# Kernel tuning notes

Measured on AMD Instinct MI355X. Metric: run time of the kernel, lower is better.

Reference implementation:

```python
import jax, jax.numpy as jnp
import numpy as np

N = 100000   # nodes
E = 1280000  # edges (avg degree ~12.8)
D = 64       # feature / hidden channels


def _init_linear(key, fan_in, fan_out):
    # Kaiming-uniform-ish init like torch Linear
    bound = 1.0 / np.sqrt(fan_in)
    return jax.random.uniform(key, (fan_in, fan_out), minval=-bound, maxval=bound)


def setup_inputs() -> dict:
    key = jax.random.key(0)
    ks = jax.random.split(key, 16)
    inp = {
        "x": jax.random.normal(ks[0], (N, D), dtype=jnp.float32),
        "edge_index": jax.random.randint(ks[1], (2, E), 0, N, dtype=jnp.int32),
        "edge_weight": jax.random.uniform(ks[2], (E,), dtype=jnp.float32),
        "batch": jnp.zeros((N,), dtype=jnp.int32),
    }
    # GraphConv params per layer: lin_rel (weight+bias) applied to aggregated
    # neighbor sum, lin_root (weight, no bias) applied to the node itself.
    for i, k in zip((1, 2, 3), range(3, 12, 3)):
        inp[f"W_rel{i}"] = _init_linear(ks[k], D, D)
        inp[f"b_rel{i}"] = jnp.zeros((D,), dtype=jnp.float32)
        inp[f"W_root{i}"] = _init_linear(ks[k + 1], D, D)
    return inp


def _graph_conv(x, src, dst, w, W_rel, b_rel, W_root):
    # message: w_ij * x_j, aggregated (sum) at target nodes
    msg = w[:, None] * x[src]                                  # [E, D]
    agg = jax.ops.segment_sum(msg, dst, num_segments=N)       # [N, D]
    return agg @ W_rel + b_rel + x @ W_root                   # [N, D]


def reference(x, edge_index, edge_weight, batch,
              W_rel1, b_rel1, W_root1,
              W_rel2, b_rel2, W_root2,
              W_rel3, b_rel3, W_root3):
    src, dst = edge_index[0], edge_index[1]
    h = jax.nn.relu(_graph_conv(x, src, dst, edge_weight, W_rel1, b_rel1, W_root1))
    h = jax.nn.relu(_graph_conv(h, src, dst, edge_weight, W_rel2, b_rel2, W_root2))
    h = _graph_conv(h, src, dst, edge_weight, W_rel3, b_rel3, W_root3)
    return h
```

## Files before the change

### kernel.cpp

```cpp
#include <hip/hip_runtime.h>
#include <hip/hip_bf16.h>

#define NN 100000
#define NE 1280000
#define DD 64
#define RSHIFT 9
#define NRANGE 196
#define NPAD (NRANGE * 512)

typedef __attribute__((ext_vector_type(8))) short bf16x8;
typedef __attribute__((ext_vector_type(4))) float f32x4;

static __device__ __forceinline__ unsigned short f2bf(float f) {
    __hip_bfloat16 h = __float2bfloat16(f);
    return *reinterpret_cast<unsigned short*>(&h);
}

__global__ __launch_bounds__(256) void f32_to_bf16_kernel(
    const float* __restrict__ in, unsigned short* __restrict__ out)
{
    int i = (blockIdx.x * 256 + threadIdx.x) * 4;
    float4 v = *(const float4*)(in + i);
    ushort4 o;
    o.x = f2bf(v.x); o.y = f2bf(v.y); o.z = f2bf(v.z); o.w = f2bf(v.w);
    *(ushort4*)(out + i) = o;
}

__global__ __launch_bounds__(256) void bpack_kernel(
    const float* __restrict__ Wrel1, const float* __restrict__ Wroot1,
    const float* __restrict__ Wrel2, const float* __restrict__ Wroot2,
    const float* __restrict__ Wrel3, const float* __restrict__ Wroot3,
    unsigned short* __restrict__ Bp)
{
    int L = blockIdx.x;
    const float* Wrel  = (L == 0) ? Wrel1  : (L == 1) ? Wrel2  : Wrel3;
    const float* Wroot = (L == 0) ? Wroot1 : (L == 1) ? Wroot2 : Wroot3;
    int tid = threadIdx.x;
    int wv = tid >> 6, lane = tid & 63, quad = lane >> 4, m16 = lane & 15;
    int n = wv * 16 + m16;
    unsigned short* o = Bp + (size_t)L * 4 * 256 * 8;
#pragma unroll
    for (int t = 0; t < 4; ++t)
#pragma unroll
        for (int j = 0; j < 8; ++j) {
            int k = t * 32 + quad * 8 + j;
            float wval = (k < 64) ? Wrel[k * 64 + n] : Wroot[(k - 64) * 64 + n];
            o[((size_t)t * 256 + tid) * 8 + j] = f2bf(wval);
        }
}

__global__ __launch_bounds__(256) void hist2_kernel(
    const int* __restrict__ dst, int* __restrict__ rangeCnt)
{
    __shared__ int h[256];
    int tid = threadIdx.x;
    h[tid] = 0;
    __syncthreads();
    int e0 = blockIdx.x * 1024 + tid * 4;
    int4 d4 = *(const int4*)(dst + e0);
    atomicAdd(&h[d4.x >> RSHIFT], 1);
    atomicAdd(&h[d4.y >> RSHIFT], 1);
    atomicAdd(&h[d4.z >> RSHIFT], 1);
    atomicAdd(&h[d4.w >> RSHIFT], 1);
    __syncthreads();
    if (tid < NRANGE && h[tid]) atomicAdd(&rangeCnt[tid], h[tid]);
}

__global__ __launch_bounds__(256) void scan196_kernel(
    const int* __restrict__ rangeCnt, int* __restrict__ rangeBase,
    int* __restrict__ gcur, int* __restrict__ rowptr)
{
    __shared__ int sd[256];
    int tid = threadIdx.x;
    int v = (tid < NRANGE) ? rangeCnt[tid] : 0;
    sd[tid] = v;
    __syncthreads();
    for (int o = 1; o < 256; o <<= 1) {
        int t = (tid >= o) ? sd[tid - o] : 0;
        __syncthreads();
        sd[tid] += t;
        __syncthreads();
    }
    if (tid < NRANGE) { int ex = sd[tid] - v; rangeBase[tid] = ex; gcur[tid] = ex; }
    if (tid == 0) { rangeBase[NRANGE] = NE; rowptr[NN] = NE; }
}

__global__ __launch_bounds__(512) void p1_bin_kernel(
    const int* __restrict__ src, const int* __restrict__ dst,
    const float* __restrict__ w, int* __restrict__ gcur,
    int2* __restrict__ ecoarse)
{
    __shared__ int2 stage[1024];
    __shared__ unsigned char sbkt[1024];
    __shared__ int cnt[256], ofs[256], gpos[256];
    __shared__ int wsum[4];

    int tid = threadIdx.x;
    int e0 = blockIdx.x * 1024 + tid * 2;
    int2   s2 = *(const int2*)(src + e0);
    int2   d2 = *(const int2*)(dst + e0);
    float2 w2 = *(const float2*)(w + e0);

    if (tid < 256) cnt[tid] = 0;
    __syncthreads();

    int ss[2] = {s2.x, s2.y};
    int dd[2] = {d2.x, d2.y};
    float ww[2] = {w2.x, w2.y};
    int b[2], p[2];
#pragma unroll
    for (int i = 0; i < 2; ++i) {
        b[i] = dd[i] >> RSHIFT;
        p[i] = atomicAdd(&cnt[b[i]], 1);
    }
    __syncthreads();

    if (tid < 256) {
        int v = cnt[tid];
        int lane6 = tid & 63;
        int sum = v;
#pragma unroll
        for (int o = 1; o < 64; o <<= 1) {
            int t = __shfl_up(sum, o);
            if (lane6 >= o) sum += t;
        }
        if (lane6 == 63) wsum[tid >> 6] = sum;
        ofs[tid] = sum - v;
    }
    __syncthreads();
    if (tid < 256) {
        int wid = tid >> 6;
        int pre = 0;
#pragma unroll
        for (int k = 0; k < 3; ++k) pre += (k < wid) ? wsum[k] : 0;
        ofs[tid] += pre;
        int cv = cnt[tid];
        if (tid < NRANGE && cv > 0) gpos[tid] = atomicAdd(&gcur[tid], cv);
    }
    __syncthreads();

#pragma unroll
    for (int i = 0; i < 2; ++i) {
        int slot = ofs[b[i]] + p[i];
        stage[slot] = make_int2(ss[i] | ((dd[i] & 511) << 17), __float_as_int(ww[i]));
        sbkt[slot] = (unsigned char)b[i];
    }
    __syncthreads();

#pragma unroll
    for (int u = 0; u < 2; ++u) {
        int j = tid + u * 512;
        int bb = sbkt[j];
        ecoarse[gpos[bb] + (j - ofs[bb])] = stage[j];
    }
}

__global__ __launch_bounds__(1024) void p2_place_kernel(
    const int2* __restrict__ ecoarse, const int* __restrict__ rangeBase,
    int* __restrict__ rowptr, int2* __restrict__ ebuf)
{
    __shared__ int cnt[512];
    __shared__ int wsum[8];
    int r = blockIdx.x, tid = threadIdx.x;
    int beg = rangeBase[r], end = rangeBase[r + 1];

    if (tid < 512) cnt[tid] = 0;
    __syncthreads();

    for (int j = beg + tid; j < end; j += 1024) {
        int2 rec = ecoarse[j];
        atomicAdd(&cnt[(rec.x >> 17) & 511], 1);
    }
    __syncthreads();

    int v = 0, sum = 0;
    if (tid < 512) {
        v = cnt[tid]; sum = v;
        int lane6 = tid & 63;
#pragma unroll
        for (int o = 1; o < 64; o <<= 1) {
            int t = __shfl_up(sum, o);
            if (lane6 >= o) sum += t;
        }
        if (lane6 == 63) wsum[tid >> 6] = sum;
    }
    __syncthreads();
    if (tid < 512) {
        int wid = tid >> 6;
        int pre = 0;
#pragma unroll
        for (int k = 0; k < 7; ++k) pre += (k < wid) ? wsum[k] : 0;
        int ex = beg + pre + sum - v;
        rowptr[(r << RSHIFT) + tid] = ex;
        cnt[tid] = ex;
    }
    __syncthreads();

    for (int j = beg + tid; j < end; j += 1024) {
        int2 rec = ecoarse[j];
        int dl = (rec.x >> 17) & 511;
        int pp = atomicAdd(&cnt[dl], 1);
        ebuf[pp] = make_int2(rec.x & 0x1FFFF, rec.y);
    }
}

template <bool RELU, bool OUT32>
__global__ __launch_bounds__(512) void fused_layer_kernel(
    const unsigned short* __restrict__ hb,
    const int* __restrict__ rowptr,
    const int2* __restrict__ ebuf,
    const unsigned short* __restrict__ Bp,
    const float* __restrict__ brel,
    void* __restrict__ outp)
{
    __shared__ __align__(16) unsigned int AstW[4 * 256];

    int tid = threadIdx.x;
    int lane = tid & 63;
    int wv = tid >> 6;
    int half = lane >> 5;
    int ch = lane & 31;
    int base = blockIdx.x * 16;
    int node = base + wv * 2 + half;

    const unsigned int* __restrict__ hw = (const unsigned int*)hb;

    bf16x8 bfrag[4];
    float bias = 0.f;
    if (wv < 4) {
#pragma unroll
        for (int t2 = 0; t2 < 4; ++t2)
            bfrag[t2] = *(const bf16x8*)(Bp + ((size_t)t2 * 256 + tid) * 8);
        bias = brel[(wv << 4) | (lane & 15)];
    }

    unsigned rootp = hw[(size_t)node * 32 + ch];

    int beg = rowptr[node];
    int end = rowptr[node + 1];
    int deg = end - beg;

    float aL[4] = {0.f, 0.f, 0.f, 0.f};
    float aH[4] = {0.f, 0.f, 0.f, 0.f};
    for (int c = 0; c < deg; c += 32) {
        int rem = deg - c;
        int nsl = rem < 32 ? rem : 32;
        int idx = (ch < nsl) ? (c + ch) : c;
        int2 e = ebuf[beg + idx];
        float wt = (ch < nsl) ? __int_as_float(e.y) : 0.f;

        for (int s0 = 0; s0 < nsl; s0 += 16) {
#pragma unroll
            for (int i = 0; i < 16; ++i) {
                int slot = s0 + i;
                bool ok = slot < nsl;
                int sl = (half << 5) | (ok ? slot : 0);
                int sr = __shfl(e.x, sl);
                float w = __shfl(wt, sl);
                w = ok ? w : 0.f;
                unsigned v = hw[(size_t)sr * 32 + ch];
                aL[i & 3] = fmaf(w, __uint_as_float(v << 16), aL[i & 3]);
                aH[i & 3] = fmaf(w, __uint_as_float(v & 0xFFFF0000u), aH[i & 3]);
            }
        }
    }
    float accL = (aL[0] + aL[1]) + (aL[2] + aL[3]);
    float accH = (aH[0] + aH[1]) + (aH[2] + aH[3]);

    int m = wv * 2 + half;
    int t = ch >> 4, q = (ch >> 2) & 3, jj = ch & 3;
    unsigned pack = ((unsigned)f2bf(accH) << 16) | (unsigned)f2bf(accL);
    AstW[t * 256 + (q * 16 + m) * 4 + jj] = pack;
    AstW[(2 + t) * 256 + (q * 16 + m) * 4 + jj] = rootp;
    __syncthreads();

    if (wv < 4) {
        int quad = lane >> 4, m16 = lane & 15;
        int n = wv * 16 + m16;
        f32x4 cacc = {0.f, 0.f, 0.f, 0.f};
#pragma unroll
        for (int t2 = 0; t2 < 4; ++t2) {
            bf16x8 a = *(const bf16x8*)&AstW[t2 * 256 + lane * 4];
            cacc = __builtin_amdgcn_mfma_f32_16x16x32_bf16(a, bfrag[t2], cacc, 0, 0, 0);
        }
#pragma unroll
        for (int reg = 0; reg < 4; ++reg) {
            int row = quad * 4 + reg;
            size_t onode = (size_t)base + row;
            float v2 = cacc[reg] + bias;
            if (RELU) v2 = fmaxf(v2, 0.f);
            if (OUT32) ((float*)outp)[onode * DD + n] = v2;
            else       ((unsigned short*)outp)[onode * DD + n] = f2bf(v2);
        }
    }
}

extern "C" void kernel_launch(void* const* d_in, const int* in_sizes, int n_in,
                              void* d_out, int out_size, void* d_ws, size_t ws_size,
                              hipStream_t stream)
{
    const float* x     = (const float*)d_in[0];
    const int*   ei    = (const int*)d_in[1];
    const float* w     = (const float*)d_in[2];
    const float* Wrel1 = (const float*)d_in[4];
    const float* brel1 = (const float*)d_in[5];
    const float* Wroot1= (const float*)d_in[6];
    const float* Wrel2 = (const float*)d_in[7];
    const float* brel2 = (const float*)d_in[8];
    const float* Wroot2= (const float*)d_in[9];
    const float* Wrel3 = (const float*)d_in[10];
    const float* brel3 = (const float*)d_in[11];
    const float* Wroot3= (const float*)d_in[12];

    float* out = (float*)d_out;

    char* ws = (char*)d_ws;
    int2*  ebuf    = (int2*)ws;                ws += (size_t)NE * 8;
    int2*  ecoarse = (int2*)ws;
    unsigned short* xb  = (unsigned short*)ws; ws += (size_t)NN * DD * 2;
    unsigned short* hb1 = (unsigned short*)ws; ws += (size_t)NN * DD * 2;
    unsigned short* hb2 = (unsigned short*)ws; ws += (size_t)NN * DD * 2;
    int*   rowptr = (int*)ws;                  ws += (size_t)(NPAD + 16) * 4;
    int*   rangeCnt  = (int*)ws;               ws += (size_t)256 * 4;
    int*   rangeBase = (int*)ws;               ws += (size_t)256 * 4;
    int*   gcur      = (int*)ws;               ws += (size_t)256 * 4;
    unsigned short* Bp = (unsigned short*)ws;

    const int* src = ei;
    const int* dst = ei + NE;

    hipMemsetAsync(rangeCnt, 0, NRANGE * 4, stream);
    bpack_kernel<<<3, 256, 0, stream>>>(Wrel1, Wroot1, Wrel2, Wroot2, Wrel3, Wroot3, Bp);
    hist2_kernel<<<1250, 256, 0, stream>>>(dst, rangeCnt);
    scan196_kernel<<<1, 256, 0, stream>>>(rangeCnt, rangeBase, gcur, rowptr);
    p1_bin_kernel<<<1250, 512, 0, stream>>>(src, dst, w, gcur, ecoarse);
    p2_place_kernel<<<NRANGE, 1024, 0, stream>>>(ecoarse, rangeBase, rowptr, ebuf);

    f32_to_bf16_kernel<<<6250, 256, 0, stream>>>(x, xb);

    fused_layer_kernel<true, false><<<NN / 16, 512, 0, stream>>>(
        xb, rowptr, ebuf, Bp, brel1, hb1);
    fused_layer_kernel<true, false><<<NN / 16, 512, 0, stream>>>(
        hb1, rowptr, ebuf, Bp + (size_t)4 * 256 * 8, brel2, hb2);
    fused_layer_kernel<false, true><<<NN / 16, 512, 0, stream>>>(
        hb2, rowptr, ebuf, Bp + (size_t)8 * 256 * 8, brel3, out);
}
```

Before: 309.0 us.

## Map one node per wave with scalar edge-record loads in fused layer

Each wave now aggregates a single node instead of two half-wave nodes, and block size grows to 1024 threads. Edge records are loaded as wave-uniform values via readfirstlane, replacing lane-distributed loads plus shuffles. This aims to cut shuffle and index overhead in the gather loop. In exchange, the upper 32 lanes do redundant work and twice as many waves are launched, which may reduce effective gather throughput.

```diff
diff --git a/kernel.cpp b/kernel.cpp
--- a/kernel.cpp
+++ b/kernel.cpp
@@ -205,7 +205,7 @@
 }
 
 template <bool RELU, bool OUT32>
-__global__ __launch_bounds__(512) void fused_layer_kernel(
+__global__ __launch_bounds__(1024) void fused_layer_kernel(
     const unsigned short* __restrict__ hb,
     const int* __restrict__ rowptr,
     const int2* __restrict__ ebuf,
@@ -218,10 +218,9 @@
     int tid = threadIdx.x;
     int lane = tid & 63;
     int wv = tid >> 6;
-    int half = lane >> 5;
     int ch = lane & 31;
     int base = blockIdx.x * 16;
-    int node = base + wv * 2 + half;
+    int node = base + wv;
 
     const unsigned int* __restrict__ hw = (const unsigned int*)hb;
 
@@ -236,42 +235,41 @@
 
     unsigned rootp = hw[(size_t)node * 32 + ch];
 
-    int beg = rowptr[node];
-    int end = rowptr[node + 1];
+    int beg = __builtin_amdgcn_readfirstlane(rowptr[node]);
+    int end = __builtin_amdgcn_readfirstlane(rowptr[node + 1]);
     int deg = end - beg;
+    const int2* __restrict__ erp = ebuf + beg;
 
     float aL[4] = {0.f, 0.f, 0.f, 0.f};
     float aH[4] = {0.f, 0.f, 0.f, 0.f};
-    for (int c = 0; c < deg; c += 32) {
-        int rem = deg - c;
-        int nsl = rem < 32 ? rem : 32;
-        int idx = (ch < nsl) ? (c + ch) : c;
-        int2 e = ebuf[beg + idx];
-        float wt = (ch < nsl) ? __int_as_float(e.y) : 0.f;
-
-        for (int s0 = 0; s0 < nsl; s0 += 16) {
-#pragma unroll
-            for (int i = 0; i < 16; ++i) {
-                int slot = s0 + i;
-                bool ok = slot < nsl;
-                int sl = (half << 5) | (ok ? slot : 0);
-                int sr = __shfl(e.x, sl);
-                float w = __shfl(wt, sl);
-                w = ok ? w : 0.f;
-                unsigned v = hw[(size_t)sr * 32 + ch];
-                aL[i & 3] = fmaf(w, __uint_as_float(v << 16), aL[i & 3]);
-                aH[i & 3] = fmaf(w, __uint_as_float(v & 0xFFFF0000u), aH[i & 3]);
-            }
+    for (int c = 0; c < deg; c += 8) {
+        int2 rec[8];
+#pragma unroll
+        for (int i = 0; i < 8; ++i) {
+            int j = c + i;
+            if (j >= deg) j = deg - 1;
+            rec[i] = erp[j];
+        }
+#pragma unroll
+        for (int i = 0; i < 8; ++i) {
+            int srcN  = __builtin_amdgcn_readfirstlane(rec[i].x);
+            int wbits = __builtin_amdgcn_readfirstlane(rec[i].y);
+            float w = (c + i < deg) ? __int_as_float(wbits) : 0.f;
+            unsigned v = hw[(size_t)srcN * 32 + ch];
+            aL[i & 3] = fmaf(w, __uint_as_float(v << 16), aL[i & 3]);
+            aH[i & 3] = fmaf(w, __uint_as_float(v & 0xFFFF0000u), aH[i & 3]);
         }
     }
     float accL = (aL[0] + aL[1]) + (aL[2] + aL[3]);
     float accH = (aH[0] + aH[1]) + (aH[2] + aH[3]);
 
-    int m = wv * 2 + half;
+    int m = wv;
     int t = ch >> 4, q = (ch >> 2) & 3, jj = ch & 3;
-    unsigned pack = ((unsigned)f2bf(accH) << 16) | (unsigned)f2bf(accL);
-    AstW[t * 256 + (q * 16 + m) * 4 + jj] = pack;
-    AstW[(2 + t) * 256 + (q * 16 + m) * 4 + jj] = rootp;
+    if (lane < 32) {
+        unsigned pack = ((unsigned)f2bf(accH) << 16) | (unsigned)f2bf(accL);
+        AstW[t * 256 + (q * 16 + m) * 4 + jj] = pack;
+        AstW[(2 + t) * 256 + (q * 16 + m) * 4 + jj] = rootp;
+    }
     __syncthreads();
 
     if (wv < 4) {
@@ -338,10 +336,10 @@
 
     f32_to_bf16_kernel<<<6250, 256, 0, stream>>>(x, xb);
 
-    fused_layer_kernel<true, false><<<NN / 16, 512, 0, stream>>>(
+    fused_layer_kernel<true, false><<<NN / 16, 1024, 0, stream>>>(
         xb, rowptr, ebuf, Bp, brel1, hb1);
-    fused_layer_kernel<true, false><<<NN / 16, 512, 0, stream>>>(
+    fused_layer_kernel<true, false><<<NN / 16, 1024, 0, stream>>>(
         hb1, rowptr, ebuf, Bp + (size_t)4 * 256 * 8, brel2, hb2);
-    fused_layer_kernel<false, true><<<NN / 16, 512, 0, stream>>>(
+    fused_layer_kernel<false, true><<<NN / 16, 1024, 0, stream>>>(
         hb2, rowptr, ebuf, Bp + (size_t)8 * 256 * 8, brel3, out);
 }
```

Result: slower. 329.5 us (+6.6%).

## Stage block edge lists in LDS and pre-scale source indices

Applied to the files above, without the earlier changes.

Each block of 16 nodes now cooperatively loads its contiguous edge records (up to 640) into shared memory, and each half-wave reads them with LDS broadcasts instead of per-chunk global loads plus cross-lane shuffles. Source indices are pre-multiplied by 32 during CSR construction so the gather address needs no multiply. Edges beyond the shared-memory capacity or leftover tails fall back to direct global reads. This adds a block barrier and extra LDS usage, which may lower occupancy.

```diff
diff --git a/kernel.cpp b/kernel.cpp
--- a/kernel.cpp
+++ b/kernel.cpp
@@ -7,6 +7,7 @@
 #define RSHIFT 9
 #define NRANGE 196
 #define NPAD (NRANGE * 512)
+#define SECAP 640
 
 typedef __attribute__((ext_vector_type(8))) short bf16x8;
 typedef __attribute__((ext_vector_type(4))) float f32x4;
@@ -200,7 +201,7 @@
         int2 rec = ecoarse[j];
         int dl = (rec.x >> 17) & 511;
         int pp = atomicAdd(&cnt[dl], 1);
-        ebuf[pp] = make_int2(rec.x & 0x1FFFF, rec.y);
+        ebuf[pp] = make_int2((rec.x & 0x1FFFF) << 5, rec.y);
     }
 }
 
@@ -214,6 +215,7 @@
     void* __restrict__ outp)
 {
     __shared__ __align__(16) unsigned int AstW[4 * 256];
+    __shared__ __align__(16) int2 se[SECAP];
 
     int tid = threadIdx.x;
     int lane = tid & 63;
@@ -225,6 +227,12 @@
 
     const unsigned int* __restrict__ hw = (const unsigned int*)hb;
 
+    int ebeg = __builtin_amdgcn_readfirstlane(rowptr[base]);
+    int eend = __builtin_amdgcn_readfirstlane(rowptr[base + 16]);
+    int ecnt = eend - ebeg;
+    int scnt = ecnt < SECAP ? ecnt : SECAP;
+    for (int j = tid; j < scnt; j += 512) se[j] = ebuf[ebeg + j];
+
     bf16x8 bfrag[4];
     float bias = 0.f;
     if (wv < 4) {
@@ -239,29 +247,38 @@
     int beg = rowptr[node];
     int end = rowptr[node + 1];
     int deg = end - beg;
+    int labeg = beg - ebeg;
+
+    __syncthreads();
 
     float aL[4] = {0.f, 0.f, 0.f, 0.f};
     float aH[4] = {0.f, 0.f, 0.f, 0.f};
-    for (int c = 0; c < deg; c += 32) {
-        int rem = deg - c;
-        int nsl = rem < 32 ? rem : 32;
-        int idx = (ch < nsl) ? (c + ch) : c;
-        int2 e = ebuf[beg + idx];
-        float wt = (ch < nsl) ? __int_as_float(e.y) : 0.f;
-
-        for (int s0 = 0; s0 < nsl; s0 += 16) {
-#pragma unroll
-            for (int i = 0; i < 16; ++i) {
-                int slot = s0 + i;
-                bool ok = slot < nsl;
-                int sl = (half << 5) | (ok ? slot : 0);
-                int sr = __shfl(e.x, sl);
-                float w = __shfl(wt, sl);
-                w = ok ? w : 0.f;
-                unsigned v = hw[(size_t)sr * 32 + ch];
-                aL[i & 3] = fmaf(w, __uint_as_float(v << 16), aL[i & 3]);
-                aH[i & 3] = fmaf(w, __uint_as_float(v & 0xFFFF0000u), aH[i & 3]);
-            }
+
+    int c = 0;
+    for (; c + 16 <= deg && labeg + c + 16 <= scnt; c += 16) {
+        int lb = labeg + c;
+        int2 rec[16];
+#pragma unroll
+        for (int i = 0; i < 16; ++i) rec[i] = se[lb + i];
+#pragma unroll
+        for (int i = 0; i < 16; ++i) {
+            float w = __int_as_float(rec[i].y);
+            unsigned v = hw[rec[i].x + ch];
+            aL[i & 3] = fmaf(w, __uint_as_float(v << 16), aL[i & 3]);
+            aH[i & 3] = fmaf(w, __uint_as_float(v & 0xFFFF0000u), aH[i & 3]);
+        }
+    }
+
+    for (; c < deg; c += 16) {
+#pragma unroll
+        for (int i = 0; i < 16; ++i) {
+            int j = c + i;
+            bool ok = j < deg;
+            int2 rec = ebuf[beg + (ok ? j : c)];
+            float w = ok ? __int_as_float(rec.y) : 0.f;
+            unsigned v = hw[rec.x + ch];
+            aL[i & 3] = fmaf(w, __uint_as_float(v << 16), aL[i & 3]);
+            aH[i & 3] = fmaf(w, __uint_as_float(v & 0xFFFF0000u), aH[i & 3]);
         }
     }
     float accL = (aL[0] + aL[1]) + (aL[2] + aL[3]);
```

Measured after the change: 446.1 us. 44.4% more time.

## Use finer 256-node bins and stage pre-scaled edge records in LDS for gather

Applied to the files above, without the earlier changes.

The coarse binning now uses 392 ranges of 256 nodes instead of 196 ranges of 512. The second placement pass runs with 512 threads per block and twice as many blocks, which raises parallelism in the CSR build. Edge source indices are stored pre-multiplied by the 128-byte row stride, and each wave stages its 32-edge chunk in shared memory instead of using two shuffles per neighbor. This removes per-edge multiply and shuffle work from the gather loop, at the cost of extra LDS traffic and more bins in the histogram and scan kernels.

```diff
diff --git a/kernel.cpp b/kernel.cpp
--- a/kernel.cpp
+++ b/kernel.cpp
@@ -4,9 +4,9 @@
 #define NN 100000
 #define NE 1280000
 #define DD 64
-#define RSHIFT 9
-#define NRANGE 196
-#define NPAD (NRANGE * 512)
+#define RSHIFT 8
+#define NRANGE 392
+#define NPAD (NRANGE * 256)
 
 typedef __attribute__((ext_vector_type(8))) short bf16x8;
 typedef __attribute__((ext_vector_type(4))) float f32x4;
@@ -49,12 +49,13 @@
         }
 }
 
-__global__ __launch_bounds__(256) void hist2_kernel(
+__global__ __launch_bounds__(256) void hist392_kernel(
     const int* __restrict__ dst, int* __restrict__ rangeCnt)
 {
-    __shared__ int h[256];
-    int tid = threadIdx.x;
-    h[tid] = 0;
+    __shared__ int h[NRANGE];
+    int tid = threadIdx.x;
+    if (tid < NRANGE) h[tid] = 0;
+    if (tid + 256 < NRANGE) h[tid + 256] = 0;
     __syncthreads();
     int e0 = blockIdx.x * 1024 + tid * 4;
     int4 d4 = *(const int4*)(dst + e0);
@@ -64,18 +65,19 @@
     atomicAdd(&h[d4.w >> RSHIFT], 1);
     __syncthreads();
     if (tid < NRANGE && h[tid]) atomicAdd(&rangeCnt[tid], h[tid]);
-}
-
-__global__ __launch_bounds__(256) void scan196_kernel(
+    if (tid + 256 < NRANGE && h[tid + 256]) atomicAdd(&rangeCnt[tid + 256], h[tid + 256]);
+}
+
+__global__ __launch_bounds__(512) void scan392_kernel(
     const int* __restrict__ rangeCnt, int* __restrict__ rangeBase,
     int* __restrict__ gcur, int* __restrict__ rowptr)
 {
-    __shared__ int sd[256];
+    __shared__ int sd[512];
     int tid = threadIdx.x;
     int v = (tid < NRANGE) ? rangeCnt[tid] : 0;
     sd[tid] = v;
     __syncthreads();
-    for (int o = 1; o < 256; o <<= 1) {
+    for (int o = 1; o < 512; o <<= 1) {
         int t = (tid >= o) ? sd[tid - o] : 0;
         __syncthreads();
         sd[tid] += t;
@@ -91,9 +93,9 @@
     int2* __restrict__ ecoarse)
 {
     __shared__ int2 stage[1024];
-    __shared__ unsigned char sbkt[1024];
-    __shared__ int cnt[256], ofs[256], gpos[256];
-    __shared__ int wsum[4];
+    __shared__ unsigned short sbkt[1024];
+    __shared__ int cnt[NRANGE], ofs[NRANGE], gpos[NRANGE];
+    __shared__ int wsum[8];
 
     int tid = threadIdx.x;
     int e0 = blockIdx.x * 1024 + tid * 2;
@@ -101,7 +103,7 @@
     int2   d2 = *(const int2*)(dst + e0);
     float2 w2 = *(const float2*)(w + e0);
 
-    if (tid < 256) cnt[tid] = 0;
+    if (tid < NRANGE) cnt[tid] = 0;
     __syncthreads();
 
     int ss[2] = {s2.x, s2.y};
@@ -115,35 +117,35 @@
     }
     __syncthreads();
 
-    if (tid < 256) {
-        int v = cnt[tid];
+    int sum = 0, v = 0;
+    if (tid < NRANGE) {
+        v = cnt[tid];
         int lane6 = tid & 63;
-        int sum = v;
+        sum = v;
 #pragma unroll
         for (int o = 1; o < 64; o <<= 1) {
             int t = __shfl_up(sum, o);
             if (lane6 >= o) sum += t;
         }
-        if (lane6 == 63) wsum[tid >> 6] = sum;
+        if (lane6 == 63 || tid == NRANGE - 1) wsum[tid >> 6] = sum;
         ofs[tid] = sum - v;
     }
     __syncthreads();
-    if (tid < 256) {
+    if (tid < NRANGE) {
         int wid = tid >> 6;
         int pre = 0;
 #pragma unroll
-        for (int k = 0; k < 3; ++k) pre += (k < wid) ? wsum[k] : 0;
+        for (int k = 0; k < 6; ++k) pre += (k < wid) ? wsum[k] : 0;
         ofs[tid] += pre;
-        int cv = cnt[tid];
-        if (tid < NRANGE && cv > 0) gpos[tid] = atomicAdd(&gcur[tid], cv);
+        if (v > 0) gpos[tid] = atomicAdd(&gcur[tid], v);
     }
     __syncthreads();
 
 #pragma unroll
     for (int i = 0; i < 2; ++i) {
         int slot = ofs[b[i]] + p[i];
-        stage[slot] = make_int2(ss[i] | ((dd[i] & 511) << 17), __float_as_int(ww[i]));
-        sbkt[slot] = (unsigned char)b[i];
+        stage[slot] = make_int2(ss[i] | ((dd[i] & 255) << 17), __float_as_int(ww[i]));
+        sbkt[slot] = (unsigned short)b[i];
     }
     __syncthreads();
 
@@ -155,26 +157,26 @@
     }
 }
 
-__global__ __launch_bounds__(1024) void p2_place_kernel(
+__global__ __launch_bounds__(512) void p2_place_kernel(
     const int2* __restrict__ ecoarse, const int* __restrict__ rangeBase,
     int* __restrict__ rowptr, int2* __restrict__ ebuf)
 {
-    __shared__ int cnt[512];
-    __shared__ int wsum[8];
+    __shared__ int cnt[256];
+    __shared__ int wsum[4];
     int r = blockIdx.x, tid = threadIdx.x;
     int beg = rangeBase[r], end = rangeBase[r + 1];
 
-    if (tid < 512) cnt[tid] = 0;
-    __syncthreads();
-
-    for (int j = beg + tid; j < end; j += 1024) {
+    if (tid < 256) cnt[tid] = 0;
+    __syncthreads();
+
+    for (int j = beg + tid; j < end; j += 512) {
         int2 rec = ecoarse[j];
-        atomicAdd(&cnt[(rec.x >> 17) & 511], 1);
+        atomicAdd(&cnt[(rec.x >> 17) & 255], 1);
     }
     __syncthreads();
 
     int v = 0, sum = 0;
-    if (tid < 512) {
+    if (tid < 256) {
         v = cnt[tid]; sum = v;
         int lane6 = tid & 63;
 #pragma unroll
@@ -185,22 +187,22 @@
         if (lane6 == 63) wsum[tid >> 6] = sum;
     }
     __syncthreads();
-    if (tid < 512) {
+    if (tid < 256) {
         int wid = tid >> 6;
         int pre = 0;
 #pragma unroll
-        for (int k = 0; k < 7; ++k) pre += (k < wid) ? wsum[k] : 0;
+        for (int k = 0; k < 3; ++k) pre += (k < wid) ? wsum[k] : 0;
         int ex = beg + pre + sum - v;
         rowptr[(r << RSHIFT) + tid] = ex;
         cnt[tid] = ex;
     }
     __syncthreads();
 
-    for (int j = beg + tid; j < end; j += 1024) {
+    for (int j = beg + tid; j < end; j += 512) {
         int2 rec = ecoarse[j];
-        int dl = (rec.x >> 17) & 511;
+        int dl = (rec.x >> 17) & 255;
         int pp = atomicAdd(&cnt[dl], 1);
-        ebuf[pp] = make_int2(rec.x & 0x1FFFF, rec.y);
+        ebuf[pp] = make_int2((rec.x & 0x1FFFF) << 7, rec.y);
     }
 }
 
@@ -214,6 +216,7 @@
     void* __restrict__ outp)
 {
     __shared__ __align__(16) unsigned int AstW[4 * 256];
+    __shared__ __align__(16) int2 seW[8][64];
 
     int tid = threadIdx.x;
     int lane = tid & 63;
@@ -223,7 +226,8 @@
     int base = blockIdx.x * 16;
     int node = base + wv * 2 + half;
 
-    const unsigned int* __restrict__ hw = (const unsigned int*)hb;
+    const char* __restrict__ hbase = (const char*)hb;
+    unsigned chB = (unsigned)ch * 4;
 
     bf16x8 bfrag[4];
     float bias = 0.f;
@@ -234,7 +238,7 @@
         bias = brel[(wv << 4) | (lane & 15)];
     }
 
-    unsigned rootp = hw[(size_t)node * 32 + ch];
+    unsigned rootp = *(const unsigned*)(hbase + (size_t)node * 128 + chB);
 
     int beg = rowptr[node];
     int end = rowptr[node + 1];
@@ -242,23 +246,22 @@
 
     float aL[4] = {0.f, 0.f, 0.f, 0.f};
     float aH[4] = {0.f, 0.f, 0.f, 0.f};
+
     for (int c = 0; c < deg; c += 32) {
-        int rem = deg - c;
-        int nsl = rem < 32 ? rem : 32;
-        int idx = (ch < nsl) ? (c + ch) : c;
-        int2 e = ebuf[beg + idx];
-        float wt = (ch < nsl) ? __int_as_float(e.y) : 0.f;
-
+        int nsl = deg - c; if (nsl > 32) nsl = 32;
+        {
+            int j = c + ch;
+            bool ok = j < deg;
+            int2 e = ebuf[beg + (ok ? j : (deg - 1))];
+            if (!ok) e.y = 0;
+            seW[wv][half * 32 + ch] = e;
+        }
         for (int s0 = 0; s0 < nsl; s0 += 16) {
 #pragma unroll
             for (int i = 0; i < 16; ++i) {
-                int slot = s0 + i;
-                bool ok = slot < nsl;
-                int sl = (half << 5) | (ok ? slot : 0);
-                int sr = __shfl(e.x, sl);
-                float w = __shfl(wt, sl);
-                w = ok ? w : 0.f;
-                unsigned v = hw[(size_t)sr * 32 + ch];
+                int2 rec = seW[wv][half * 32 + s0 + i];
+                float w = __int_as_float(rec.y);
+                unsigned v = *(const unsigned*)(hbase + ((unsigned)rec.x + chB));
                 aL[i & 3] = fmaf(w, __uint_as_float(v << 16), aL[i & 3]);
                 aH[i & 3] = fmaf(w, __uint_as_float(v & 0xFFFF0000u), aH[i & 3]);
             }
@@ -321,9 +324,9 @@
     unsigned short* hb1 = (unsigned short*)ws; ws += (size_t)NN * DD * 2;
     unsigned short* hb2 = (unsigned short*)ws; ws += (size_t)NN * DD * 2;
     int*   rowptr = (int*)ws;                  ws += (size_t)(NPAD + 16) * 4;
-    int*   rangeCnt  = (int*)ws;               ws += (size_t)256 * 4;
-    int*   rangeBase = (int*)ws;               ws += (size_t)256 * 4;
-    int*   gcur      = (int*)ws;               ws += (size_t)256 * 4;
+    int*   rangeCnt  = (int*)ws;               ws += (size_t)512 * 4;
+    int*   rangeBase = (int*)ws;               ws += (size_t)512 * 4;
+    int*   gcur      = (int*)ws;               ws += (size_t)512 * 4;
     unsigned short* Bp = (unsigned short*)ws;
 
     const int* src = ei;
@@ -331,10 +334,10 @@
 
     hipMemsetAsync(rangeCnt, 0, NRANGE * 4, stream);
     bpack_kernel<<<3, 256, 0, stream>>>(Wrel1, Wroot1, Wrel2, Wroot2, Wrel3, Wroot3, Bp);
-    hist2_kernel<<<1250, 256, 0, stream>>>(dst, rangeCnt);
-    scan196_kernel<<<1, 256, 0, stream>>>(rangeCnt, rangeBase, gcur, rowptr);
+    hist392_kernel<<<1250, 256, 0, stream>>>(dst, rangeCnt);
+    scan392_kernel<<<1, 512, 0, stream>>>(rangeCnt, rangeBase, gcur, rowptr);
     p1_bin_kernel<<<1250, 512, 0, stream>>>(src, dst, w, gcur, ecoarse);
-    p2_place_kernel<<<NRANGE, 1024, 0, stream>>>(ecoarse, rangeBase, rowptr, ebuf);
+    p2_place_kernel<<<NRANGE, 512, 0, stream>>>(ecoarse, rangeBase, rowptr, ebuf);
 
     f32_to_bf16_kernel<<<6250, 256, 0, stream>>>(x, xb);
 
```

Result: faster. 289.2 us (-6.4%).
